# Kernel optimization log

Hardware: AMD Instinct MI355X
Metric: run time of the kernel (lower is better)

The kernel has to match this reference:

```python
import jax, jax.numpy as jnp
import numpy as np

N_HEADS = 8
D_HEAD = 64
INNER = N_HEADS * D_HEAD  # 512
D_X = 512
D_CTX = 768

def setup_inputs() -> dict:
    key = jax.random.key(0)
    ks = jax.random.split(key, 7)
    x = jax.random.normal(ks[0], (4, 4096, D_X), dtype=jnp.float32)
    context = jax.random.normal(ks[1], (4, 1024, D_CTX), dtype=jnp.float32)
    # Glorot-ish scaled params
    Wq = jax.random.normal(ks[2], (D_X, INNER), dtype=jnp.float32) / np.sqrt(D_X)
    Wk = jax.random.normal(ks[3], (D_CTX, INNER), dtype=jnp.float32) / np.sqrt(D_CTX)
    Wv = jax.random.normal(ks[4], (D_CTX, INNER), dtype=jnp.float32) / np.sqrt(D_CTX)
    Wo = jax.random.normal(ks[5], (INNER, INNER), dtype=jnp.float32) / np.sqrt(INNER)
    bo = jnp.zeros((INNER,), dtype=jnp.float32)
    return {"x": x, "context": context, "Wq": Wq, "Wk": Wk, "Wv": Wv, "Wo": Wo, "bo": bo}

def reference(x, context, Wq, Wk, Wv, Wo, bo):
    B, Nq, _ = x.shape
    Nc = context.shape[1]
    scale = D_HEAD ** -0.5
    # QKV projections (no bias), reshape to heads: b s (h d) -> b h s d
    q = (x @ Wq).reshape(B, Nq, N_HEADS, D_HEAD).transpose(0, 2, 1, 3)
    k = (context @ Wk).reshape(B, Nc, N_HEADS, D_HEAD).transpose(0, 2, 1, 3)
    v = (context @ Wv).reshape(B, Nc, N_HEADS, D_HEAD).transpose(0, 2, 1, 3)
    # scores: [B, H, Nq, Nc]
    score = jnp.einsum('bhqd,bhkd->bhqk', q, k) * scale
    weights = jax.nn.softmax(score, axis=-1)
    attn = jnp.einsum('bhqk,bhkd->bhqd', weights, v)
    out = attn.transpose(0, 2, 1, 3).reshape(B, Nq, INNER)
    return out @ Wo + bo
```

## Files before the change

kernel.cpp:

```cpp
#include <hip/hip_runtime.h>
#include <math.h>

typedef __attribute__((ext_vector_type(8))) short s8v;
typedef __attribute__((ext_vector_type(4))) float f4v;
typedef unsigned short u16;
typedef unsigned int u32;

constexpr int Bsz = 4, NQ = 4096, NC = 1024, NH = 8, DH = 64, DI = 512, DC = 768;

__device__ __forceinline__ u16 f2bf(float f) {
  union { float f; u32 u; } v; v.f = f;
  u32 r = v.u + 0x7fff + ((v.u >> 16) & 1);
  return (u16)(r >> 16);
}

__device__ __forceinline__ u32 pack2(float a, float b) {
  union { float f; u32 u; } ua, ub; ua.f = a; ub.f = b;
#if __has_builtin(__builtin_amdgcn_perm)
  return __builtin_amdgcn_perm(ub.u + 0x8000u, ua.u + 0x8000u, 0x07060302u);
#else
  return ((ub.u + 0x8000u) & 0xffff0000u) | ((ua.u + 0x8000u) >> 16);
#endif
}

__device__ __forceinline__ u32 cvtpk(float a, float b) {
  u32 r;
  asm("v_cvt_pk_bf16_f32 %0, %1, %2" : "=v"(r) : "v"(a), "v"(b));
  return r;
}

#if __has_builtin(__builtin_amdgcn_exp2f)
#define EXP2(x) __builtin_amdgcn_exp2f(x)
#else
#define EXP2(x) exp2f(x)
#endif

__device__ __forceinline__ void g2l16(const void* g, void* l) {
  __builtin_amdgcn_global_load_lds((const __attribute__((address_space(1))) u32*)g,
                                   (__attribute__((address_space(3))) u32*)l, 16, 0, 0);
}

__global__ __launch_bounds__(256) void prep(const float* __restrict__ Wq, const float* __restrict__ Wk,
                                            const float* __restrict__ Wv, const float* __restrict__ Wo,
                                            u16* __restrict__ wqT, u16* __restrict__ wkvT,
                                            u16* __restrict__ woT) {
  int idx = blockIdx.x;
  int z = idx / 96, rem = idx % 96, kx = rem % 12, ny = rem / 12;
  const float* src; u16* dst; int K; const int N = 512;
  if (z == 0)      { src = Wq; dst = wqT;              K = 512; }
  else if (z == 1) { src = Wk; dst = wkvT;             K = 768; }
  else if (z == 2) { src = Wv; dst = wkvT + 512 * 768; K = 768; }
  else             { src = Wo; dst = woT;              K = 512; }
  int k0 = kx * 64, n0 = ny * 64;
  if (k0 >= K) return;
  __shared__ u16 t[64][65];
  int tid = threadIdx.x, jr = tid & 63, ir = tid >> 6;
  for (int it = 0; it < 16; ++it) { int i = it * 4 + ir; t[i][jr] = f2bf(src[(size_t)(k0 + i) * N + n0 + jr]); }
  __syncthreads();
  for (int it = 0; it < 16; ++it) { int i = it * 4 + ir; dst[(size_t)(n0 + i) * K + k0 + jr] = t[jr][i]; }
}

template <int MODE, bool F32A>
__device__ __forceinline__ void gemm_body(const void* __restrict__ Av, const u16* __restrict__ Bt,
                                          void* __restrict__ C0, void* __restrict__ C1,
                                          const float* __restrict__ bias, int N, int K,
                                          float oscale, int nbx, int mby,
                                          u16* Al, u16* Bl) {
  int mb = mby * 128, nb = nbx * 128;
  int tid = threadIdx.x, lane = tid & 63, quad = lane >> 4, l16 = lane & 15, wave = tid >> 6;
  int wm = (wave >> 1) * 64, wn = (wave & 1) * 64;
  f4v acc[4][4];
  #pragma unroll
  for (int i = 0; i < 4; i++)
    #pragma unroll
    for (int j = 0; j < 4; j++) acc[i][j] = (f4v){0.f, 0.f, 0.f, 0.f};

  int r0 = tid >> 2;
  int cs = ((tid & 3) ^ ((r0 >> 1) & 3)) * 8;
  int lin = tid * 8;
  const u16* Bp0 = Bt + (size_t)(nb + r0) * K + cs;
  const u16* Bp1 = Bt + (size_t)(nb + r0 + 64) * K + cs;
  const float* Af0 = nullptr; const float* Af1 = nullptr;
  const u16* Ap0 = nullptr; const u16* Ap1 = nullptr;
  if constexpr (F32A) {
    Af0 = (const float*)Av + (size_t)(mb + r0) * K + cs;
    Af1 = Af0 + (size_t)64 * K;
  } else {
    Ap0 = (const u16*)Av + (size_t)(mb + r0) * K + cs;
    Ap1 = Ap0 + (size_t)64 * K;
  }
  float4 a00, a01, a10, a11;

#define BSTAGE(k0, buf) do { u16* bl_ = Bl + (buf) * 4096; \
    g2l16(Bp0 + (k0), bl_ + lin); g2l16(Bp1 + (k0), bl_ + lin + 2048); } while (0)
#define ASTAGE_G(k0, buf) do { u16* al_ = Al + (buf) * 4096; \
    g2l16(Ap0 + (k0), al_ + lin); g2l16(Ap1 + (k0), al_ + lin + 2048); } while (0)
#define ALOAD(k0) do { \
    a00 = *(const float4*)(Af0 + (k0)); a01 = *(const float4*)(Af0 + (k0) + 4); \
    a10 = *(const float4*)(Af1 + (k0)); a11 = *(const float4*)(Af1 + (k0) + 4); } while (0)
#define AWRITE(buf) do { u16* al_ = Al + (buf) * 4096; \
    union { u32 d[4]; s8v v; } ua, ub; \
    ua.d[0] = cvtpk(a00.x, a00.y); ua.d[1] = cvtpk(a00.z, a00.w); \
    ua.d[2] = cvtpk(a01.x, a01.y); ua.d[3] = cvtpk(a01.z, a01.w); \
    ub.d[0] = cvtpk(a10.x, a10.y); ub.d[1] = cvtpk(a10.z, a10.w); \
    ub.d[2] = cvtpk(a11.x, a11.y); ub.d[3] = cvtpk(a11.z, a11.w); \
    *(s8v*)(al_ + lin) = ua.v; *(s8v*)(al_ + lin + 2048) = ub.v; } while (0)

  if constexpr (F32A) { ALOAD(0); BSTAGE(0, 0); AWRITE(0); }
  else { ASTAGE_G(0, 0); BSTAGE(0, 0); }

  int nk = K >> 5;
  int swq8 = (quad ^ ((l16 >> 1) & 3)) * 8;
  for (int t = 0; t < nk; ++t) {
    __syncthreads();
    int nxt = (t + 1) * 32, nbuf = (t + 1) & 1;
    if (t + 1 < nk) {
      if constexpr (F32A) ALOAD(nxt); else ASTAGE_G(nxt, nbuf);
      BSTAGE(nxt, nbuf);
    }
    const u16* al = Al + (t & 1) * 4096;
    const u16* bl = Bl + (t & 1) * 4096;
    s8v af[4], bfr[4];
    #pragma unroll
    for (int i = 0; i < 4; i++) af[i] = *(const s8v*)(al + (wm + i * 16 + l16) * 32 + swq8);
    #pragma unroll
    for (int j = 0; j < 4; j++) bfr[j] = *(const s8v*)(bl + (wn + j * 16 + l16) * 32 + swq8);
    #pragma unroll
    for (int i = 0; i < 4; i++)
      #pragma unroll
      for (int j = 0; j < 4; j++)
        acc[i][j] = __builtin_amdgcn_mfma_f32_16x16x32_bf16(af[i], bfr[j], acc[i][j], 0, 0, 0);
    if constexpr (F32A) { if (t + 1 < nk) AWRITE(nbuf); }
  }
#undef BSTAGE
#undef ASTAGE_G
#undef ALOAD
#undef AWRITE
  #pragma unroll
  for (int i = 0; i < 4; i++) {
    int rbase = mb + wm + i * 16 + quad * 4;
    #pragma unroll
    for (int j = 0; j < 4; j++) {
      int col = nb + wn + j * 16 + l16;
      if (MODE == 0) {
        u16* Cb = (u16*)C0;
        #pragma unroll
        for (int r = 0; r < 4; r++) Cb[(size_t)(rbase + r) * N + col] = f2bf(acc[i][j][r] * oscale);
      } else if (MODE == 1) {
        float* Cf = (float*)C0;
        #pragma unroll
        for (int r = 0; r < 4; r++) Cf[(size_t)(rbase + r) * N + col] = acc[i][j][r] + bias[col];
      } else {
        if (col < 512) {
          u16* Kb = (u16*)C0;
          #pragma unroll
          for (int r = 0; r < 4; r++) Kb[(size_t)(rbase + r) * 512 + col] = f2bf(acc[i][j][r]);
        } else {
          u16* Vt = (u16*)C1;
          int hd = col - 512, h = hd >> 6, d = hd & 63;
          int bb = rbase >> 10, tl = rbase & 1023;
          int tbase = tl & ~63, a0 = tl & 63;
          int pb = (a0 & 32) + ((a0 & 15) >> 2) * 8 + (((a0 >> 4) & 1) << 2);
          uint2 ov;
          ov.x = pack2(acc[i][j][0], acc[i][j][1]);
          ov.y = pack2(acc[i][j][2], acc[i][j][3]);
          *(uint2*)(Vt + ((size_t)(bb * NH + h) * DH + d) * NC + tbase + pb) = ov;
        }
      }
    }
  }
}

__global__ __launch_bounds__(256, 3) void proj_all(const float* __restrict__ x, const float* __restrict__ ctx,
                                                   const u16* __restrict__ wqT, const u16* __restrict__ wkvT,
                                                   u16* __restrict__ Qb, u16* __restrict__ Kb,
                                                   u16* __restrict__ Vtb, float qscale) {
  __shared__ alignas(16) u16 Al[2][128][32];
  __shared__ alignas(16) u16 Bl[2][128][32];
  int bx = blockIdx.x;
  if (bx < 256) {
    gemm_body<2, true>(ctx, wkvT, Kb, Vtb, nullptr, 1024, 768, 1.0f, bx & 7, bx >> 3,
                       (u16*)Al, (u16*)Bl);
  } else {
    int bi = bx - 256;
    gemm_body<0, true>(x, wqT, Qb, nullptr, nullptr, 512, 512, qscale, bi & 3, bi >> 2,
                       (u16*)Al, (u16*)Bl);
  }
}

__global__ __launch_bounds__(256, 2) void outproj(const u16* __restrict__ Ob, const u16* __restrict__ woT,
                                                  float* __restrict__ out, const float* __restrict__ bo) {
  __shared__ alignas(16) u16 Al[2][128][32];
  __shared__ alignas(16) u16 Bl[2][128][32];
  gemm_body<1, false>(Ob, woT, out, nullptr, bo, 512, 512, 1.0f, blockIdx.x, blockIdx.y,
                      (u16*)Al, (u16*)Bl);
}

__global__ __launch_bounds__(256, 4) void attn(const u16* __restrict__ Q, const u16* __restrict__ Kb,
                                               const u16* __restrict__ Vt, u16* __restrict__ O) {
  __shared__ alignas(16) u16 Kl[2][64][64];
  __shared__ alignas(16) u16 Vl[2][64][64];
  int qt = blockIdx.x, h = blockIdx.y, b = blockIdx.z;
  int tid = threadIdx.x, wave = tid >> 6, lane = tid & 63, quad = lane >> 4, l16 = lane & 15;
  int q0 = qt * 128 + wave * 32;
  int x7 = l16 & 7;

  int kr = tid >> 3, kc = (tid & 7) ^ (kr & 7);
  const u16* kg = Kb + ((size_t)b * NC + kr) * 512 + h * DH + kc * 8;
  const u16* vg = Vt + ((size_t)(b * NH + h) * DH + kr) * NC + kc * 8;

#define ASTAGE(kt, buf) do { \
    const u16* kg_ = kg + (size_t)(kt) * 64 * 512; \
    const u16* vg_ = vg + (kt) * 64; \
    u16* kl_ = (u16*)Kl + (buf) * 4096; u16* vl_ = (u16*)Vl + (buf) * 4096; \
    g2l16(kg_,            kl_ + tid * 8); \
    g2l16(kg_ + 32 * 512, kl_ + (tid + 256) * 8); \
    g2l16(vg_,            vl_ + tid * 8); \
    g2l16(vg_ + 32 * NC,  vl_ + (tid + 256) * 8); } while (0)

  s8v aq[2][2];
  {
    const u16* Qp = Q + ((size_t)b * NQ + q0 + l16) * DI + h * DH + quad * 8;
    #pragma unroll
    for (int n = 0; n < 2; n++) {
      aq[n][0] = *(const s8v*)(Qp + (size_t)n * 16 * DI);
      aq[n][1] = *(const s8v*)(Qp + (size_t)n * 16 * DI + 32);
    }
  }
  s8v vones;
  #pragma unroll
  for (int i = 0; i < 8; i++) vones[i] = (short)0x3F80;

  f4v oacc[4][2];
  f4v lacc[2];
  #pragma unroll
  for (int d = 0; d < 4; d++)
    #pragma unroll
    for (int n = 0; n < 2; n++) oacc[d][n] = (f4v){0.f, 0.f, 0.f, 0.f};
  #pragma unroll
  for (int n = 0; n < 2; n++) lacc[n] = (f4v){0.f, 0.f, 0.f, 0.f};

  ASTAGE(0, 0);
  for (int kt = 0; kt < NC / 64; ++kt) {
    int buf = kt & 1;
    __syncthreads();
    if (kt + 1 < NC / 64) ASTAGE(kt + 1, buf ^ 1);
    const u16* kb = (const u16*)Kl + buf * 4096;
    const u16* vb = (const u16*)Vl + buf * 4096;

    f4v S0[2][2], S1[2][2];
    #pragma unroll
    for (int mi = 0; mi < 2; mi++)
      #pragma unroll
      for (int n = 0; n < 2; n++) { S0[mi][n] = (f4v){0.f,0.f,0.f,0.f}; S1[mi][n] = (f4v){0.f,0.f,0.f,0.f}; }
    __builtin_amdgcn_s_setprio(1);
    #pragma unroll
    for (int cd = 0; cd < 2; cd++) {
      int ch = ((4 * cd + quad) ^ x7) * 8;
      s8v k00 = *(const s8v*)(kb + (l16     ) * 64 + ch);
      s8v k01 = *(const s8v*)(kb + (l16 + 16) * 64 + ch);
      #pragma unroll
      for (int n = 0; n < 2; n++) {
        S0[0][n] = __builtin_amdgcn_mfma_f32_16x16x32_bf16(k00, aq[n][cd], S0[0][n], 0, 0, 0);
        S0[1][n] = __builtin_amdgcn_mfma_f32_16x16x32_bf16(k01, aq[n][cd], S0[1][n], 0, 0, 0);
      }
      s8v k10 = *(const s8v*)(kb + (l16 + 32) * 64 + ch);
      s8v k11 = *(const s8v*)(kb + (l16 + 48) * 64 + ch);
      #pragma unroll
      for (int n = 0; n < 2; n++) {
        S1[0][n] = __builtin_amdgcn_mfma_f32_16x16x32_bf16(k10, aq[n][cd], S1[0][n], 0, 0, 0);
        S1[1][n] = __builtin_amdgcn_mfma_f32_16x16x32_bf16(k11, aq[n][cd], S1[1][n], 0, 0, 0);
      }
    }
    __builtin_amdgcn_s_setprio(0);

    s8v pf0[2];
    #pragma unroll
    for (int n = 0; n < 2; n++) {
      float p00 = EXP2(S0[0][n][0]), p01 = EXP2(S0[0][n][1]), p02 = EXP2(S0[0][n][2]), p03 = EXP2(S0[0][n][3]);
      float p10 = EXP2(S0[1][n][0]), p11 = EXP2(S0[1][n][1]), p12 = EXP2(S0[1][n][2]), p13 = EXP2(S0[1][n][3]);
      union { u32 d[4]; s8v v; } u;
      u.d[0] = cvtpk(p00, p01); u.d[1] = cvtpk(p02, p03);
      u.d[2] = cvtpk(p10, p11); u.d[3] = cvtpk(p12, p13);
      pf0[n] = u.v;
    }
    __builtin_amdgcn_s_setprio(1);
    #pragma unroll
    for (int n = 0; n < 2; n++)
      lacc[n] = __builtin_amdgcn_mfma_f32_16x16x32_bf16(vones, pf0[n], lacc[n], 0, 0, 0);
    #pragma unroll
    for (int d = 0; d < 4; d++) {
      int ch = (quad ^ x7) * 8;
      s8v vf = *(const s8v*)(vb + (d * 16 + l16) * 64 + ch);
      #pragma unroll
      for (int n = 0; n < 2; n++)
        oacc[d][n] = __builtin_amdgcn_mfma_f32_16x16x32_bf16(vf, pf0[n], oacc[d][n], 0, 0, 0);
    }
    __builtin_amdgcn_s_setprio(0);

    s8v pf1[2];
    #pragma unroll
    for (int n = 0; n < 2; n++) {
      float p00 = EXP2(S1[0][n][0]), p01 = EXP2(S1[0][n][1]), p02 = EXP2(S1[0][n][2]), p03 = EXP2(S1[0][n][3]);
      float p10 = EXP2(S1[1][n][0]), p11 = EXP2(S1[1][n][1]), p12 = EXP2(S1[1][n][2]), p13 = EXP2(S1[1][n][3]);
      union { u32 d[4]; s8v v; } u;
      u.d[0] = cvtpk(p00, p01); u.d[1] = cvtpk(p02, p03);
      u.d[2] = cvtpk(p10, p11); u.d[3] = cvtpk(p12, p13);
      pf1[n] = u.v;
    }
    __builtin_amdgcn_s_setprio(1);
    #pragma unroll
    for (int n = 0; n < 2; n++)
      lacc[n] = __builtin_amdgcn_mfma_f32_16x16x32_bf16(vones, pf1[n], lacc[n], 0, 0, 0);
    #pragma unroll
    for (int d = 0; d < 4; d++) {
      int ch = ((4 + quad) ^ x7) * 8;
      s8v vf = *(const s8v*)(vb + (d * 16 + l16) * 64 + ch);
      #pragma unroll
      for (int n = 0; n < 2; n++)
        oacc[d][n] = __builtin_amdgcn_mfma_f32_16x16x32_bf16(vf, pf1[n], oacc[d][n], 0, 0, 0);
    }
    __builtin_amdgcn_s_setprio(0);
  }
#undef ASTAGE

  float inv[2];
  #pragma unroll
  for (int n = 0; n < 2; n++) inv[n] = 1.0f / lacc[n][0];

  #pragma unroll
  for (int d = 0; d < 4; d++)
    #pragma unroll
    for (int n = 0; n < 2; n++) {
      int q = q0 + n * 16 + l16;
      uint2 ov;
      ov.x = cvtpk(oacc[d][n][0] * inv[n], oacc[d][n][1] * inv[n]);
      ov.y = cvtpk(oacc[d][n][2] * inv[n], oacc[d][n][3] * inv[n]);
      *(uint2*)(O + ((size_t)b * NQ + q) * DI + h * DH + d * 16 + quad * 4) = ov;
    }
}

extern "C" void kernel_launch(void* const* d_in, const int* in_sizes, int n_in,
                              void* d_out, int out_size, void* d_ws, size_t ws_size,
                              hipStream_t stream) {
  const float* x   = (const float*)d_in[0];
  const float* ctx = (const float*)d_in[1];
  const float* Wq  = (const float*)d_in[2];
  const float* Wk  = (const float*)d_in[3];
  const float* Wv  = (const float*)d_in[4];
  const float* Wo  = (const float*)d_in[5];
  const float* bo  = (const float*)d_in[6];
  float* out = (float*)d_out;

  u16* w    = (u16*)d_ws;
  u16* wqT  = w;
  u16* wkvT = wqT  + 262144;
  u16* woT  = wkvT + 786432;
  u16* Qb   = woT  + 262144;
  u16* Kbuf = Qb   + 8388608;
  u16* Vtb  = Kbuf + 2097152;
  u16* Ob   = Vtb  + 2097152;

  const float qscale = 0.125f * 1.44269504f;

  prep<<<384, 256, 0, stream>>>(Wq, Wk, Wv, Wo, wqT, wkvT, woT);
  proj_all<<<768, 256, 0, stream>>>(x, ctx, wqT, wkvT, Qb, Kbuf, Vtb, qscale);
  attn<<<dim3(32, 8, 4), 256, 0, stream>>>(Qb, Kbuf, Vtb, Ob);
  outproj<<<dim3(4, 128), 256, 0, stream>>>(Ob, woT, out, bo);
}
```

Before: 194.3 us.

## Triple-buffer GEMM LDS staging with explicit waitcnt and XCD-aware block remap

The shared GEMM body moves from double to triple-buffered LDS staging. Loads are issued two k-steps ahead, and the loop uses a single barrier per iteration with hand-set vmcnt/lgkmcnt waits instead of __syncthreads, so global latency hides behind more MFMA work. The projection and output-projection kernels also remap block indices so that neighbouring tiles land on the same XCD for better L2 reuse, and outproj's launch bounds go from 2 to 3 blocks per CU. The hand-written vmcnt counts depend on the number of outstanding loads per stage, so any later change to the staging code could silently introduce race conditions, and the larger LDS footprint may reduce occupancy.

```diff
diff --git a/kernel.cpp b/kernel.cpp
--- a/kernel.cpp
+++ b/kernel.cpp
@@ -79,7 +79,7 @@
   int cs = ((tid & 3) ^ ((r0 >> 1) & 3)) * 8;
   int lin = tid * 8;
   const u16* Bp0 = Bt + (size_t)(nb + r0) * K + cs;
-  const u16* Bp1 = Bt + (size_t)(nb + r0 + 64) * K + cs;
+  const u16* Bp1 = Bp0 + (size_t)64 * K;
   const float* Af0 = nullptr; const float* Af1 = nullptr;
   const u16* Ap0 = nullptr; const u16* Ap1 = nullptr;
   if constexpr (F32A) {
@@ -89,53 +89,76 @@
     Ap0 = (const u16*)Av + (size_t)(mb + r0) * K + cs;
     Ap1 = Ap0 + (size_t)64 * K;
   }
-  float4 a00, a01, a10, a11;
-
-#define BSTAGE(k0, buf) do { u16* bl_ = Bl + (buf) * 4096; \
-    g2l16(Bp0 + (k0), bl_ + lin); g2l16(Bp1 + (k0), bl_ + lin + 2048); } while (0)
-#define ASTAGE_G(k0, buf) do { u16* al_ = Al + (buf) * 4096; \
-    g2l16(Ap0 + (k0), al_ + lin); g2l16(Ap1 + (k0), al_ + lin + 2048); } while (0)
-#define ALOAD(k0) do { \
-    a00 = *(const float4*)(Af0 + (k0)); a01 = *(const float4*)(Af0 + (k0) + 4); \
-    a10 = *(const float4*)(Af1 + (k0)); a11 = *(const float4*)(Af1 + (k0) + 4); } while (0)
-#define AWRITE(buf) do { u16* al_ = Al + (buf) * 4096; \
-    union { u32 d[4]; s8v v; } ua, ub; \
-    ua.d[0] = cvtpk(a00.x, a00.y); ua.d[1] = cvtpk(a00.z, a00.w); \
-    ua.d[2] = cvtpk(a01.x, a01.y); ua.d[3] = cvtpk(a01.z, a01.w); \
-    ub.d[0] = cvtpk(a10.x, a10.y); ub.d[1] = cvtpk(a10.z, a10.w); \
-    ub.d[2] = cvtpk(a11.x, a11.y); ub.d[3] = cvtpk(a11.z, a11.w); \
-    *(s8v*)(al_ + lin) = ua.v; *(s8v*)(al_ + lin + 2048) = ub.v; } while (0)
-
-  if constexpr (F32A) { ALOAD(0); BSTAGE(0, 0); AWRITE(0); }
-  else { ASTAGE_G(0, 0); BSTAGE(0, 0); }
+  float4 ra[4], rb[4];
+
+#define BSTG(k0, bl_) do { g2l16(Bp0 + (k0), (bl_) + lin); g2l16(Bp1 + (k0), (bl_) + lin + 2048); } while (0)
+#define ASTG(k0, al_) do { g2l16(Ap0 + (k0), (al_) + lin); g2l16(Ap1 + (k0), (al_) + lin + 2048); } while (0)
+#define ALD(k0, s) do { \
+    s[0] = *(const float4*)(Af0 + (k0)); s[1] = *(const float4*)(Af0 + (k0) + 4); \
+    s[2] = *(const float4*)(Af1 + (k0)); s[3] = *(const float4*)(Af1 + (k0) + 4); } while (0)
+#define AWR(s, al_) do { union { u32 d[4]; s8v v; } ua, ub; \
+    ua.d[0] = cvtpk(s[0].x, s[0].y); ua.d[1] = cvtpk(s[0].z, s[0].w); \
+    ua.d[2] = cvtpk(s[1].x, s[1].y); ua.d[3] = cvtpk(s[1].z, s[1].w); \
+    ub.d[0] = cvtpk(s[2].x, s[2].y); ub.d[1] = cvtpk(s[2].z, s[2].w); \
+    ub.d[2] = cvtpk(s[3].x, s[3].y); ub.d[3] = cvtpk(s[3].z, s[3].w); \
+    *(s8v*)((al_) + lin) = ua.v; *(s8v*)((al_) + lin + 2048) = ub.v; } while (0)
+
+  u16 *Ar = Al, *Aw = Al + 4096, *As = Al + 8192;
+  u16 *Br = Bl, *Bw = Bl + 4096, *Bs = Bl + 8192;
+  if constexpr (F32A) {
+    ALD(0, ra); BSTG(0, Br); AWR(ra, Ar);
+    ALD(32, rb); BSTG(32, Bw);
+  } else {
+    ASTG(0, Ar); BSTG(0, Br);
+    ASTG(32, Aw); BSTG(32, Bw);
+  }
 
   int nk = K >> 5;
   int swq8 = (quad ^ ((l16 >> 1) & 3)) * 8;
   for (int t = 0; t < nk; ++t) {
-    __syncthreads();
-    int nxt = (t + 1) * 32, nbuf = (t + 1) & 1;
     if (t + 1 < nk) {
-      if constexpr (F32A) ALOAD(nxt); else ASTAGE_G(nxt, nbuf);
-      BSTAGE(nxt, nbuf);
-    }
-    const u16* al = Al + (t & 1) * 4096;
-    const u16* bl = Bl + (t & 1) * 4096;
+      if constexpr (F32A) asm volatile("s_waitcnt vmcnt(6) lgkmcnt(0)" ::: "memory");
+      else                asm volatile("s_waitcnt vmcnt(4) lgkmcnt(0)" ::: "memory");
+    } else {
+      asm volatile("s_waitcnt vmcnt(0) lgkmcnt(0)" ::: "memory");
+    }
+    __builtin_amdgcn_s_barrier();
+    asm volatile("" ::: "memory");
+    __builtin_amdgcn_sched_barrier(0);
+
+    if (t + 2 < nk) {
+      int nxt = (t + 2) * 32;
+      if constexpr (F32A) {
+        if (t & 1) { ALD(nxt, rb); } else { ALD(nxt, ra); }
+        BSTG(nxt, Bs);
+      } else {
+        ASTG(nxt, As); BSTG(nxt, Bs);
+      }
+    }
+
     s8v af[4], bfr[4];
     #pragma unroll
-    for (int i = 0; i < 4; i++) af[i] = *(const s8v*)(al + (wm + i * 16 + l16) * 32 + swq8);
-    #pragma unroll
-    for (int j = 0; j < 4; j++) bfr[j] = *(const s8v*)(bl + (wn + j * 16 + l16) * 32 + swq8);
+    for (int i = 0; i < 4; i++) af[i] = *(const s8v*)(Ar + (wm + i * 16 + l16) * 32 + swq8);
+    #pragma unroll
+    for (int j = 0; j < 4; j++) bfr[j] = *(const s8v*)(Br + (wn + j * 16 + l16) * 32 + swq8);
     #pragma unroll
     for (int i = 0; i < 4; i++)
       #pragma unroll
       for (int j = 0; j < 4; j++)
         acc[i][j] = __builtin_amdgcn_mfma_f32_16x16x32_bf16(af[i], bfr[j], acc[i][j], 0, 0, 0);
-    if constexpr (F32A) { if (t + 1 < nk) AWRITE(nbuf); }
-  }
-#undef BSTAGE
-#undef ASTAGE_G
-#undef ALOAD
-#undef AWRITE
+
+    if constexpr (F32A) {
+      if (t + 1 < nk) {
+        if (t & 1) { AWR(ra, Aw); } else { AWR(rb, Aw); }
+      }
+    }
+    u16* tA = Ar; Ar = Aw; Aw = As; As = tA;
+    u16* tB = Br; Br = Bw; Bw = Bs; Bs = tB;
+  }
+#undef BSTG
+#undef ASTG
+#undef ALD
+#undef AWR
   #pragma unroll
   for (int i = 0; i < 4; i++) {
     int rbase = mb + wm + i * 16 + quad * 4;
@@ -175,24 +198,28 @@
                                                    const u16* __restrict__ wqT, const u16* __restrict__ wkvT,
                                                    u16* __restrict__ Qb, u16* __restrict__ Kb,
                                                    u16* __restrict__ Vtb, float qscale) {
-  __shared__ alignas(16) u16 Al[2][128][32];
-  __shared__ alignas(16) u16 Bl[2][128][32];
+  __shared__ alignas(16) u16 Al[3][128][32];
+  __shared__ alignas(16) u16 Bl[3][128][32];
   int bx = blockIdx.x;
-  if (bx < 256) {
-    gemm_body<2, true>(ctx, wkvT, Kb, Vtb, nullptr, 1024, 768, 1.0f, bx & 7, bx >> 3,
+  int xcd = bx & 7, off = bx >> 3;
+  if (off < 32) {
+    int bi = xcd * 32 + off;
+    gemm_body<2, true>(ctx, wkvT, Kb, Vtb, nullptr, 1024, 768, 1.0f, bi & 7, bi >> 3,
                        (u16*)Al, (u16*)Bl);
   } else {
-    int bi = bx - 256;
+    int bi = xcd * 64 + (off - 32);
     gemm_body<0, true>(x, wqT, Qb, nullptr, nullptr, 512, 512, qscale, bi & 3, bi >> 2,
                        (u16*)Al, (u16*)Bl);
   }
 }
 
-__global__ __launch_bounds__(256, 2) void outproj(const u16* __restrict__ Ob, const u16* __restrict__ woT,
+__global__ __launch_bounds__(256, 3) void outproj(const u16* __restrict__ Ob, const u16* __restrict__ woT,
                                                   float* __restrict__ out, const float* __restrict__ bo) {
-  __shared__ alignas(16) u16 Al[2][128][32];
-  __shared__ alignas(16) u16 Bl[2][128][32];
-  gemm_body<1, false>(Ob, woT, out, nullptr, bo, 512, 512, 1.0f, blockIdx.x, blockIdx.y,
+  __shared__ alignas(16) u16 Al[3][128][32];
+  __shared__ alignas(16) u16 Bl[3][128][32];
+  int bx = blockIdx.x;
+  int idx = (bx & 7) * 64 + (bx >> 3);
+  gemm_body<1, false>(Ob, woT, out, nullptr, bo, 512, 512, 1.0f, idx & 3, idx >> 2,
                       (u16*)Al, (u16*)Bl);
 }
 
@@ -366,5 +393,5 @@
   prep<<<384, 256, 0, stream>>>(Wq, Wk, Wv, Wo, wqT, wkvT, woT);
   proj_all<<<768, 256, 0, stream>>>(x, ctx, wqT, wkvT, Qb, Kbuf, Vtb, qscale);
   attn<<<dim3(32, 8, 4), 256, 0, stream>>>(Qb, Kbuf, Vtb, Ob);
-  outproj<<<dim3(4, 128), 256, 0, stream>>>(Ob, woT, out, bo);
-}
+  outproj<<<512, 256, 0, stream>>>(Ob, woT, out, bo);
+}
```

After: 188.6 us. 2.9% less time.

## Halve GEMM M-tile to 64 rows and remap blocks across XCDs

Applied to the files above, without the earlier changes.

Shrinks the projection and output-projection GEMM tiles from 128x128 to 64x128, which doubles the block count and reduces per-block registers and LDS so occupancy can rise to 4 blocks per CU. It also remaps linear block indices so that consecutive tiles sharing A rows land on the same XCD, aiming for better L2 reuse. The aim is better latency hiding and load balance across CUs on these small GEMMs. The cost is lower arithmetic intensity per tile, with more B-tile traffic per output element.

```diff
diff --git a/kernel.cpp b/kernel.cpp
--- a/kernel.cpp
+++ b/kernel.cpp
@@ -66,12 +66,12 @@
                                           const float* __restrict__ bias, int N, int K,
                                           float oscale, int nbx, int mby,
                                           u16* Al, u16* Bl) {
-  int mb = mby * 128, nb = nbx * 128;
+  int mb = mby * 64, nb = nbx * 128;
   int tid = threadIdx.x, lane = tid & 63, quad = lane >> 4, l16 = lane & 15, wave = tid >> 6;
-  int wm = (wave >> 1) * 64, wn = (wave & 1) * 64;
-  f4v acc[4][4];
-  #pragma unroll
-  for (int i = 0; i < 4; i++)
+  int wm = (wave >> 1) * 32, wn = (wave & 1) * 64;
+  f4v acc[2][4];
+  #pragma unroll
+  for (int i = 0; i < 2; i++)
     #pragma unroll
     for (int j = 0; j < 4; j++) acc[i][j] = (f4v){0.f, 0.f, 0.f, 0.f};
 
@@ -79,65 +79,56 @@
   int cs = ((tid & 3) ^ ((r0 >> 1) & 3)) * 8;
   int lin = tid * 8;
   const u16* Bp0 = Bt + (size_t)(nb + r0) * K + cs;
-  const u16* Bp1 = Bt + (size_t)(nb + r0 + 64) * K + cs;
-  const float* Af0 = nullptr; const float* Af1 = nullptr;
-  const u16* Ap0 = nullptr; const u16* Ap1 = nullptr;
-  if constexpr (F32A) {
-    Af0 = (const float*)Av + (size_t)(mb + r0) * K + cs;
-    Af1 = Af0 + (size_t)64 * K;
-  } else {
-    Ap0 = (const u16*)Av + (size_t)(mb + r0) * K + cs;
-    Ap1 = Ap0 + (size_t)64 * K;
-  }
-  float4 a00, a01, a10, a11;
-
-#define BSTAGE(k0, buf) do { u16* bl_ = Bl + (buf) * 4096; \
-    g2l16(Bp0 + (k0), bl_ + lin); g2l16(Bp1 + (k0), bl_ + lin + 2048); } while (0)
-#define ASTAGE_G(k0, buf) do { u16* al_ = Al + (buf) * 4096; \
-    g2l16(Ap0 + (k0), al_ + lin); g2l16(Ap1 + (k0), al_ + lin + 2048); } while (0)
-#define ALOAD(k0) do { \
-    a00 = *(const float4*)(Af0 + (k0)); a01 = *(const float4*)(Af0 + (k0) + 4); \
-    a10 = *(const float4*)(Af1 + (k0)); a11 = *(const float4*)(Af1 + (k0) + 4); } while (0)
-#define AWRITE(buf) do { u16* al_ = Al + (buf) * 4096; \
-    union { u32 d[4]; s8v v; } ua, ub; \
-    ua.d[0] = cvtpk(a00.x, a00.y); ua.d[1] = cvtpk(a00.z, a00.w); \
-    ua.d[2] = cvtpk(a01.x, a01.y); ua.d[3] = cvtpk(a01.z, a01.w); \
-    ub.d[0] = cvtpk(a10.x, a10.y); ub.d[1] = cvtpk(a10.z, a10.w); \
-    ub.d[2] = cvtpk(a11.x, a11.y); ub.d[3] = cvtpk(a11.z, a11.w); \
-    *(s8v*)(al_ + lin) = ua.v; *(s8v*)(al_ + lin + 2048) = ub.v; } while (0)
-
-  if constexpr (F32A) { ALOAD(0); BSTAGE(0, 0); AWRITE(0); }
-  else { ASTAGE_G(0, 0); BSTAGE(0, 0); }
+  const u16* Bp1 = Bp0 + (size_t)64 * K;
+  const float* Af0 = nullptr;
+  const u16* Ap0 = nullptr;
+  if constexpr (F32A) Af0 = (const float*)Av + (size_t)(mb + r0) * K + cs;
+  else                Ap0 = (const u16*)Av + (size_t)(mb + r0) * K + cs;
+  float4 ra[2];
+
+#define BSTG(k0, bl_) do { g2l16(Bp0 + (k0), (bl_) + lin); g2l16(Bp1 + (k0), (bl_) + lin + 2048); } while (0)
+#define ASTG(k0, al_) do { g2l16(Ap0 + (k0), (al_) + lin); } while (0)
+#define ALD(k0) do { ra[0] = *(const float4*)(Af0 + (k0)); ra[1] = *(const float4*)(Af0 + (k0) + 4); } while (0)
+#define AWR(al_) do { union { u32 d[4]; s8v v; } ua; \
+    ua.d[0] = cvtpk(ra[0].x, ra[0].y); ua.d[1] = cvtpk(ra[0].z, ra[0].w); \
+    ua.d[2] = cvtpk(ra[1].x, ra[1].y); ua.d[3] = cvtpk(ra[1].z, ra[1].w); \
+    *(s8v*)((al_) + lin) = ua.v; } while (0)
+
+  if constexpr (F32A) { ALD(0); BSTG(0, Bl); AWR(Al); }
+  else { ASTG(0, Al); BSTG(0, Bl); }
 
   int nk = K >> 5;
   int swq8 = (quad ^ ((l16 >> 1) & 3)) * 8;
   for (int t = 0; t < nk; ++t) {
     __syncthreads();
-    int nxt = (t + 1) * 32, nbuf = (t + 1) & 1;
+    int cur = t & 1, nxtb = cur ^ 1;
     if (t + 1 < nk) {
-      if constexpr (F32A) ALOAD(nxt); else ASTAGE_G(nxt, nbuf);
-      BSTAGE(nxt, nbuf);
-    }
-    const u16* al = Al + (t & 1) * 4096;
-    const u16* bl = Bl + (t & 1) * 4096;
-    s8v af[4], bfr[4];
-    #pragma unroll
-    for (int i = 0; i < 4; i++) af[i] = *(const s8v*)(al + (wm + i * 16 + l16) * 32 + swq8);
-    #pragma unroll
-    for (int j = 0; j < 4; j++) bfr[j] = *(const s8v*)(bl + (wn + j * 16 + l16) * 32 + swq8);
-    #pragma unroll
-    for (int i = 0; i < 4; i++)
+      int nxt = (t + 1) * 32;
+      if constexpr (F32A) ALD(nxt); else ASTG(nxt, Al + nxtb * 2048);
+      BSTG(nxt, Bl + nxtb * 4096);
+    }
+    const u16* ar = Al + cur * 2048;
+    const u16* br = Bl + cur * 4096;
+    s8v af[2], bfr[4];
+    #pragma unroll
+    for (int i = 0; i < 2; i++) af[i] = *(const s8v*)(ar + (wm + i * 16 + l16) * 32 + swq8);
+    #pragma unroll
+    for (int j = 0; j < 4; j++) bfr[j] = *(const s8v*)(br + (wn + j * 16 + l16) * 32 + swq8);
+    #pragma unroll
+    for (int i = 0; i < 2; i++)
       #pragma unroll
       for (int j = 0; j < 4; j++)
         acc[i][j] = __builtin_amdgcn_mfma_f32_16x16x32_bf16(af[i], bfr[j], acc[i][j], 0, 0, 0);
-    if constexpr (F32A) { if (t + 1 < nk) AWRITE(nbuf); }
-  }
-#undef BSTAGE
-#undef ASTAGE_G
-#undef ALOAD
-#undef AWRITE
-  #pragma unroll
-  for (int i = 0; i < 4; i++) {
+    if constexpr (F32A) {
+      if (t + 1 < nk) AWR(Al + nxtb * 2048);
+    }
+  }
+#undef BSTG
+#undef ASTG
+#undef ALD
+#undef AWR
+  #pragma unroll
+  for (int i = 0; i < 2; i++) {
     int rbase = mb + wm + i * 16 + quad * 4;
     #pragma unroll
     for (int j = 0; j < 4; j++) {
@@ -171,28 +162,32 @@
   }
 }
 
-__global__ __launch_bounds__(256, 3) void proj_all(const float* __restrict__ x, const float* __restrict__ ctx,
+__global__ __launch_bounds__(256, 4) void proj_all(const float* __restrict__ x, const float* __restrict__ ctx,
                                                    const u16* __restrict__ wqT, const u16* __restrict__ wkvT,
                                                    u16* __restrict__ Qb, u16* __restrict__ Kb,
                                                    u16* __restrict__ Vtb, float qscale) {
-  __shared__ alignas(16) u16 Al[2][128][32];
+  __shared__ alignas(16) u16 Al[2][64][32];
   __shared__ alignas(16) u16 Bl[2][128][32];
   int bx = blockIdx.x;
-  if (bx < 256) {
-    gemm_body<2, true>(ctx, wkvT, Kb, Vtb, nullptr, 1024, 768, 1.0f, bx & 7, bx >> 3,
+  int xcd = bx & 7, off = bx >> 3;
+  if (off < 64) {
+    int bi = xcd * 64 + off;
+    gemm_body<2, true>(ctx, wkvT, Kb, Vtb, nullptr, 1024, 768, 1.0f, bi & 7, bi >> 3,
                        (u16*)Al, (u16*)Bl);
   } else {
-    int bi = bx - 256;
+    int bi = xcd * 128 + (off - 64);
     gemm_body<0, true>(x, wqT, Qb, nullptr, nullptr, 512, 512, qscale, bi & 3, bi >> 2,
                        (u16*)Al, (u16*)Bl);
   }
 }
 
-__global__ __launch_bounds__(256, 2) void outproj(const u16* __restrict__ Ob, const u16* __restrict__ woT,
+__global__ __launch_bounds__(256, 4) void outproj(const u16* __restrict__ Ob, const u16* __restrict__ woT,
                                                   float* __restrict__ out, const float* __restrict__ bo) {
-  __shared__ alignas(16) u16 Al[2][128][32];
+  __shared__ alignas(16) u16 Al[2][64][32];
   __shared__ alignas(16) u16 Bl[2][128][32];
-  gemm_body<1, false>(Ob, woT, out, nullptr, bo, 512, 512, 1.0f, blockIdx.x, blockIdx.y,
+  int bx = blockIdx.x;
+  int idx = (bx & 7) * 128 + (bx >> 3);
+  gemm_body<1, false>(Ob, woT, out, nullptr, bo, 512, 512, 1.0f, idx & 3, idx >> 2,
                       (u16*)Al, (u16*)Bl);
 }
 
@@ -364,7 +359,7 @@
   const float qscale = 0.125f * 1.44269504f;
 
   prep<<<384, 256, 0, stream>>>(Wq, Wk, Wv, Wo, wqT, wkvT, woT);
-  proj_all<<<768, 256, 0, stream>>>(x, ctx, wqT, wkvT, Qb, Kbuf, Vtb, qscale);
+  proj_all<<<1536, 256, 0, stream>>>(x, ctx, wqT, wkvT, Qb, Kbuf, Vtb, qscale);
   attn<<<dim3(32, 8, 4), 256, 0, stream>>>(Qb, Kbuf, Vtb, Ob);
-  outproj<<<dim3(4, 128), 256, 0, stream>>>(Ob, woT, out, bo);
-}
+  outproj<<<1024, 256, 0, stream>>>(Ob, woT, out, bo);
+}
```

Result: no change. 192.2 us (-1.1%).
